# Kernel tuning notes

Hardware: AMD Instinct MI355X
Metric: run time of the kernel (lower is better)

## Reference

```python
import jax, jax.numpy as jnp
import numpy as np
from jax import lax

N, D, H, E = 8192, 1024, 4096, 8


def setup_inputs() -> dict:
    key = jax.random.key(0)
    ks = jax.random.split(key, 7)
    s = 0.02
    return {
        "x": jax.random.normal(ks[0], (N, D), dtype=jnp.float32),
        "Wr": jax.random.normal(ks[1], (E, D), dtype=jnp.float32) * s,
        "br": jnp.zeros((E,), dtype=jnp.float32),
        "Wup": jax.random.normal(ks[2], (E, H, D), dtype=jnp.float32) * s,
        "bup": jnp.zeros((E, H), dtype=jnp.float32),
        "Wdown": jax.random.normal(ks[3], (E, D, H), dtype=jnp.float32) * s,
        "bdown": jnp.zeros((E, D), dtype=jnp.float32),
    }


def reference(x, Wr, br, Wup, bup, Wdown, bdown):
    # Router: softmax over logits; only argmax is used (softmax is monotone,
    # argmax of softmax == argmax of logits).
    logits = x @ Wr.T + br            # [N, E]
    scores = jax.nn.softmax(logits, axis=-1)
    top1 = jnp.argmax(scores, axis=-1)  # [N] int

    out0 = jnp.zeros_like(x)

    def body(out, ew):
        i, Wu, bu, Wd, bd = ew
        h = jax.nn.silu(x @ Wu.T + bu)   # [N, H]
        y = h @ Wd.T + bd                # [N, D]
        out = jnp.where((top1 == i)[:, None], y, out)
        return out, None

    idx = jnp.arange(Wup.shape[0])
    out, _ = lax.scan(body, out0, (idx, Wup, bup, Wdown, bdown))
    return out
```

## Files before the change

### kernel.cpp

```cpp
#include <hip/hip_runtime.h>

#define NT 8192
#define DD 1024
#define HH 4096
#define EE 8

typedef __attribute__((ext_vector_type(8))) short short8;
typedef __attribute__((ext_vector_type(4))) float f32x4;

__device__ __forceinline__ unsigned short f2bf(float f) {
    unsigned int u = __float_as_uint(f);
    u += 0x7FFFu + ((u >> 16) & 1u);
    return (unsigned short)(u >> 16);
}

__device__ __forceinline__ void gload_lds16(const void* g, void* l) {
    __builtin_amdgcn_global_load_lds(
        (const __attribute__((address_space(1))) unsigned int*)g,
        (__attribute__((address_space(3))) unsigned int*)l, 16, 0, 0);
}

__global__ __launch_bounds__(256) void cvtw_kernel(const float* __restrict__ a,
                                                   const float* __restrict__ b,
                                                   unsigned short* __restrict__ da,
                                                   unsigned short* __restrict__ db) {
    const size_t half = (size_t)EE * HH * DD;
    size_t i = ((size_t)blockIdx.x * 256 + threadIdx.x) * 4;
    const float* s; unsigned short* d;
    if (i < half) { s = a + i; d = da + i; }
    else          { s = b + (i - half); d = db + (i - half); }
    float4 v = *(const float4*)s;
    ushort4 o;
    o.x = f2bf(v.x); o.y = f2bf(v.y); o.z = f2bf(v.z); o.w = f2bf(v.w);
    *(ushort4*)d = o;
}

__global__ __launch_bounds__(256) void router_kernel(const float* __restrict__ x,
                                                     const float* __restrict__ Wr,
                                                     const float* __restrict__ br,
                                                     int* __restrict__ counts,
                                                     int* __restrict__ tlist) {
    __shared__ float sW[EE * DD];
    const int t = threadIdx.x;
    for (int i = t; i < EE * DD / 4; i += 256)
        ((float4*)sW)[i] = ((const float4*)Wr)[i];
    __syncthreads();
    const int lane = t & 63;
    const int wv = t >> 6;
    const int token = blockIdx.x * 4 + wv;
    const float* xr = x + (size_t)token * DD;
    float acc[EE];
#pragma unroll
    for (int e = 0; e < EE; e++) acc[e] = 0.f;
    for (int k = lane; k < DD; k += 64) {
        float xv = xr[k];
#pragma unroll
        for (int e = 0; e < EE; e++) acc[e] += xv * sW[e * DD + k];
    }
#pragma unroll
    for (int off = 32; off > 0; off >>= 1) {
#pragma unroll
        for (int e = 0; e < EE; e++) acc[e] += __shfl_xor(acc[e], off);
    }
    if (lane == 0) {
        int best = 0;
        float bv = acc[0] + br[0];
#pragma unroll
        for (int e = 1; e < EE; e++) {
            float v = acc[e] + br[e];
            if (v > bv) { bv = v; best = e; }
        }
        int pos = atomicAdd(&counts[best], 1);
        tlist[best * NT + pos] = token;
    }
}

__global__ __launch_bounds__(256) void gather_kernel(const float* __restrict__ x,
                                                     const int* __restrict__ tlist,
                                                     const int* __restrict__ counts,
                                                     unsigned short* __restrict__ xg) {
    const int row = blockIdx.x * 4 + (threadIdx.x >> 6);
    const int lane = threadIdx.x & 63;
    int off[EE];
    int s = 0;
#pragma unroll
    for (int k = 0; k < EE; k++) { off[k] = s; s += counts[k]; }
    int e = 0;
#pragma unroll
    for (int k = 1; k < EE; k++)
        if (row >= off[k]) e = k;
    const int token = tlist[e * NT + row - off[e]];
    const float4* src = (const float4*)(x + (size_t)token * DD);
    ushort4* dst = (ushort4*)(xg + (size_t)row * DD);
#pragma unroll
    for (int it = 0; it < 4; it++) {
        float4 v = src[it * 64 + lane];
        ushort4 o;
        o.x = f2bf(v.x); o.y = f2bf(v.y); o.z = f2bf(v.z); o.w = f2bf(v.w);
        dst[it * 64 + lane] = o;
    }
}


__global__ __launch_bounds__(256) void up_gemm(const unsigned short* __restrict__ xg,
                                               const unsigned short* __restrict__ Wub,
                                               const float* __restrict__ bup,
                                               const int* __restrict__ counts,
                                               unsigned short* __restrict__ hbuf) {
    const int e = blockIdx.z;
    int off_e = 0, cnt;
    {
        int s = 0;
#pragma unroll
        for (int k = 0; k < EE; k++) { if (k == e) off_e = s; s += counts[k]; }
        cnt = counts[e];
    }
    const int m0 = blockIdx.y * 128;
    if (m0 >= cnt) return;
    const int n0 = blockIdx.x * 128;
    const int t = threadIdx.x;

    __shared__ unsigned short sA[128 * 32];
    __shared__ unsigned short sB[128 * 32];

    const int r0 = t >> 2;
    const int kc = (t & 3) ^ ((r0 >> 1) & 3);
    const int c1 = cnt - 1;
    int ra = m0 + r0;      if (ra > c1) ra = c1;
    int rb = m0 + 64 + r0; if (rb > c1) rb = c1;
    const unsigned short* gA0 = xg + (size_t)(off_e + ra) * DD + kc * 8;
    const unsigned short* gA1 = xg + (size_t)(off_e + rb) * DD + kc * 8;
    const unsigned short* gB0 = Wub + ((size_t)e * HH + n0 + r0) * DD + kc * 8;
    const unsigned short* gB1 = Wub + ((size_t)e * HH + n0 + 64 + r0) * DD + kc * 8;
    unsigned short* lA0 = sA + t * 8;
    unsigned short* lA1 = sA + (t + 256) * 8;
    unsigned short* lB0 = sB + t * 8;
    unsigned short* lB1 = sB + (t + 256) * 8;

    const int lane = t & 63;
    const int wm = ((t >> 6) & 1) * 64;
    const int wn = (t >> 7) * 64;
    const int mrow = lane & 15;
    const int kq = lane >> 4;
    const int slot = (kq ^ ((mrow >> 1) & 3)) * 8;

    f32x4 acc[4][4];
#pragma unroll
    for (int i = 0; i < 4; i++)
#pragma unroll
        for (int j = 0; j < 4; j++)
            acc[i][j] = (f32x4){0.f, 0.f, 0.f, 0.f};

    for (int kt = 0; kt < DD; kt += 32) {
        __syncthreads();
        gload_lds16(gA0 + kt, lA0);
        gload_lds16(gA1 + kt, lA1);
        gload_lds16(gB0 + kt, lB0);
        gload_lds16(gB1 + kt, lB1);
        __syncthreads();
        short8 a[4], b[4];
#pragma unroll
        for (int i = 0; i < 4; i++) {
            a[i] = *(const short8*)(sA + (wm + i * 16 + mrow) * 32 + slot);
            b[i] = *(const short8*)(sB + (wn + i * 16 + mrow) * 32 + slot);
        }
#pragma unroll
        for (int i = 0; i < 4; i++)
#pragma unroll
            for (int j = 0; j < 4; j++)
                acc[i][j] = __builtin_amdgcn_mfma_f32_16x16x32_bf16(a[i], b[j], acc[i][j], 0, 0, 0);
    }

    float bias[4];
#pragma unroll
    for (int j = 0; j < 4; j++) bias[j] = bup[e * HH + n0 + wn + j * 16 + mrow];
#pragma unroll
    for (int i = 0; i < 4; i++) {
#pragma unroll
        for (int r = 0; r < 4; r++) {
            int m = m0 + wm + i * 16 + kq * 4 + r;
            if (m < cnt) {
                unsigned short* hrow = hbuf + (size_t)(off_e + m) * HH + n0 + wn + mrow;
#pragma unroll
                for (int j = 0; j < 4; j++) {
                    float v = acc[i][j][r] + bias[j];
                    v = v / (1.f + __expf(-v));
                    hrow[j * 16] = f2bf(v);
                }
            }
        }
    }
}

__global__ __launch_bounds__(256) void down_gemm(const unsigned short* __restrict__ hbuf,
                                                 const unsigned short* __restrict__ Wdb,
                                                 const float* __restrict__ bdown,
                                                 const int* __restrict__ counts,
                                                 const int* __restrict__ tlist,
                                                 float* __restrict__ out) {
    const int e = blockIdx.z;
    int off_e = 0, cnt;
    {
        int s = 0;
#pragma unroll
        for (int k = 0; k < EE; k++) { if (k == e) off_e = s; s += counts[k]; }
        cnt = counts[e];
    }
    const int m0 = blockIdx.y * 128;
    if (m0 >= cnt) return;
    const int n0 = blockIdx.x * 128;
    const int t = threadIdx.x;

    __shared__ unsigned short sA[128 * 32];
    __shared__ unsigned short sB[128 * 32];

    const int r0 = t >> 2;
    const int kc = (t & 3) ^ ((r0 >> 1) & 3);
    const int c1 = cnt - 1;
    int ra = m0 + r0;      if (ra > c1) ra = c1;
    int rb = m0 + 64 + r0; if (rb > c1) rb = c1;
    const unsigned short* gA0 = hbuf + (size_t)(off_e + ra) * HH + kc * 8;
    const unsigned short* gA1 = hbuf + (size_t)(off_e + rb) * HH + kc * 8;
    const unsigned short* gB0 = Wdb + ((size_t)e * DD + n0 + r0) * HH + kc * 8;
    const unsigned short* gB1 = Wdb + ((size_t)e * DD + n0 + 64 + r0) * HH + kc * 8;
    unsigned short* lA0 = sA + t * 8;
    unsigned short* lA1 = sA + (t + 256) * 8;
    unsigned short* lB0 = sB + t * 8;
    unsigned short* lB1 = sB + (t + 256) * 8;

    const int lane = t & 63;
    const int wm = ((t >> 6) & 1) * 64;
    const int wn = (t >> 7) * 64;
    const int mrow = lane & 15;
    const int kq = lane >> 4;
    const int slot = (kq ^ ((mrow >> 1) & 3)) * 8;

    f32x4 acc[4][4];
#pragma unroll
    for (int i = 0; i < 4; i++)
#pragma unroll
        for (int j = 0; j < 4; j++)
            acc[i][j] = (f32x4){0.f, 0.f, 0.f, 0.f};

    for (int kt = 0; kt < HH; kt += 32) {
        __syncthreads();
        gload_lds16(gA0 + kt, lA0);
        gload_lds16(gA1 + kt, lA1);
        gload_lds16(gB0 + kt, lB0);
        gload_lds16(gB1 + kt, lB1);
        __syncthreads();
        short8 a[4], b[4];
#pragma unroll
        for (int i = 0; i < 4; i++) {
            a[i] = *(const short8*)(sA + (wm + i * 16 + mrow) * 32 + slot);
            b[i] = *(const short8*)(sB + (wn + i * 16 + mrow) * 32 + slot);
        }
#pragma unroll
        for (int i = 0; i < 4; i++)
#pragma unroll
            for (int j = 0; j < 4; j++)
                acc[i][j] = __builtin_amdgcn_mfma_f32_16x16x32_bf16(a[i], b[j], acc[i][j], 0, 0, 0);
    }

    const int* tl = tlist + e * NT;
    float bias[4];
#pragma unroll
    for (int j = 0; j < 4; j++) bias[j] = bdown[e * DD + n0 + wn + j * 16 + mrow];
#pragma unroll
    for (int i = 0; i < 4; i++) {
#pragma unroll
        for (int r = 0; r < 4; r++) {
            int m = m0 + wm + i * 16 + kq * 4 + r;
            if (m < cnt) {
                int token = tl[m];
                float* orow = out + (size_t)token * DD + n0 + wn + mrow;
#pragma unroll
                for (int j = 0; j < 4; j++)
                    orow[j * 16] = acc[i][j][r] + bias[j];
            }
        }
    }
}

extern "C" void kernel_launch(void* const* d_in, const int* in_sizes, int n_in,
                              void* d_out, int out_size, void* d_ws, size_t ws_size,
                              hipStream_t stream) {
    const float* x     = (const float*)d_in[0];
    const float* Wr    = (const float*)d_in[1];
    const float* br    = (const float*)d_in[2];
    const float* Wup   = (const float*)d_in[3];
    const float* bup   = (const float*)d_in[4];
    const float* Wdown = (const float*)d_in[5];
    const float* bdown = (const float*)d_in[6];
    float* out = (float*)d_out;

    char* w = (char*)d_ws;
    int* counts  = (int*)w;               w += 256;
    int* tlist   = (int*)w;               w += (size_t)EE * NT * 4;
    unsigned short* xg   = (unsigned short*)w;  w += (size_t)NT * DD * 2;
    unsigned short* hbuf = (unsigned short*)w;  w += (size_t)NT * HH * 2;
    unsigned short* Wub  = (unsigned short*)w;  w += (size_t)EE * HH * DD * 2;
    unsigned short* Wdb  = (unsigned short*)w;

    hipMemsetAsync(counts, 0, EE * sizeof(int), stream);

    cvtw_kernel<<<(2 * (size_t)EE * HH * DD) / 1024, 256, 0, stream>>>(Wup, Wdown, Wub, Wdb);
    router_kernel<<<NT / 4, 256, 0, stream>>>(x, Wr, br, counts, tlist);
    gather_kernel<<<NT / 4, 256, 0, stream>>>(x, tlist, counts, xg);

    dim3 gu(HH / 128, NT / 128, EE);
    up_gemm<<<gu, 256, 0, stream>>>(xg, Wub, bup, counts, hbuf);
    dim3 gd(DD / 128, NT / 128, EE);
    down_gemm<<<gd, 256, 0, stream>>>(hbuf, Wdb, bdown, counts, tlist, out);
}
```

Measured before the change: 659.0 us.

## Fuse fp32-to-bf16 weight conversion into GEMM loads and split-K the down GEMM

```diff
diff --git a/kernel.cpp b/kernel.cpp
--- a/kernel.cpp
+++ b/kernel.cpp
@@ -20,19 +20,13 @@
         (__attribute__((address_space(3))) unsigned int*)l, 16, 0, 0);
 }
 
-__global__ __launch_bounds__(256) void cvtw_kernel(const float* __restrict__ a,
-                                                   const float* __restrict__ b,
-                                                   unsigned short* __restrict__ da,
-                                                   unsigned short* __restrict__ db) {
-    const size_t half = (size_t)EE * HH * DD;
-    size_t i = ((size_t)blockIdx.x * 256 + threadIdx.x) * 4;
-    const float* s; unsigned short* d;
-    if (i < half) { s = a + i; d = da + i; }
-    else          { s = b + (i - half); d = db + (i - half); }
-    float4 v = *(const float4*)s;
-    ushort4 o;
-    o.x = f2bf(v.x); o.y = f2bf(v.y); o.z = f2bf(v.z); o.w = f2bf(v.w);
-    *(ushort4*)d = o;
+__device__ __forceinline__ void pack_store8(unsigned short* l, float4 a, float4 b) {
+    uint4 w;
+    w.x = (unsigned)f2bf(a.x) | ((unsigned)f2bf(a.y) << 16);
+    w.y = (unsigned)f2bf(a.z) | ((unsigned)f2bf(a.w) << 16);
+    w.z = (unsigned)f2bf(b.x) | ((unsigned)f2bf(b.y) << 16);
+    w.w = (unsigned)f2bf(b.z) | ((unsigned)f2bf(b.w) << 16);
+    *(uint4*)l = w;
 }
 
 __global__ __launch_bounds__(256) void router_kernel(const float* __restrict__ x,
@@ -103,7 +97,7 @@
 
 
 __global__ __launch_bounds__(256) void up_gemm(const unsigned short* __restrict__ xg,
-                                               const unsigned short* __restrict__ Wub,
+                                               const float* __restrict__ Wup,
                                                const float* __restrict__ bup,
                                                const int* __restrict__ counts,
                                                unsigned short* __restrict__ hbuf) {
@@ -124,18 +118,20 @@
     __shared__ unsigned short sB[128 * 32];
 
     const int r0 = t >> 2;
-    const int kc = (t & 3) ^ ((r0 >> 1) & 3);
+    const int kc = t & 3;
+    const int ksw = (r0 >> 1) & 3;
+    const int kcA = kc ^ ksw;
     const int c1 = cnt - 1;
     int ra = m0 + r0;      if (ra > c1) ra = c1;
     int rb = m0 + 64 + r0; if (rb > c1) rb = c1;
-    const unsigned short* gA0 = xg + (size_t)(off_e + ra) * DD + kc * 8;
-    const unsigned short* gA1 = xg + (size_t)(off_e + rb) * DD + kc * 8;
-    const unsigned short* gB0 = Wub + ((size_t)e * HH + n0 + r0) * DD + kc * 8;
-    const unsigned short* gB1 = Wub + ((size_t)e * HH + n0 + 64 + r0) * DD + kc * 8;
+    const unsigned short* gA0 = xg + (size_t)(off_e + ra) * DD + kcA * 8;
+    const unsigned short* gA1 = xg + (size_t)(off_e + rb) * DD + kcA * 8;
+    const float* gB0 = Wup + ((size_t)e * HH + n0 + r0) * DD + kc * 8;
+    const float* gB1 = Wup + ((size_t)e * HH + n0 + 64 + r0) * DD + kc * 8;
     unsigned short* lA0 = sA + t * 8;
     unsigned short* lA1 = sA + (t + 256) * 8;
-    unsigned short* lB0 = sB + t * 8;
-    unsigned short* lB1 = sB + (t + 256) * 8;
+    unsigned short* lB0 = sB + (r0 * 4 + (kc ^ ksw)) * 8;
+    unsigned short* lB1 = sB + ((r0 + 64) * 4 + (kc ^ ksw)) * 8;
 
     const int lane = t & 63;
     const int wm = ((t >> 6) & 1) * 64;
@@ -152,11 +148,15 @@
             acc[i][j] = (f32x4){0.f, 0.f, 0.f, 0.f};
 
     for (int kt = 0; kt < DD; kt += 32) {
+        float4 b00 = *(const float4*)(gB0 + kt);
+        float4 b01 = *(const float4*)(gB0 + kt + 4);
+        float4 b10 = *(const float4*)(gB1 + kt);
+        float4 b11 = *(const float4*)(gB1 + kt + 4);
         __syncthreads();
         gload_lds16(gA0 + kt, lA0);
         gload_lds16(gA1 + kt, lA1);
-        gload_lds16(gB0 + kt, lB0);
-        gload_lds16(gB1 + kt, lB1);
+        pack_store8(lB0, b00, b01);
+        pack_store8(lB1, b10, b11);
         __syncthreads();
         short8 a[4], b[4];
 #pragma unroll
@@ -193,12 +193,11 @@
 }
 
 __global__ __launch_bounds__(256) void down_gemm(const unsigned short* __restrict__ hbuf,
-                                                 const unsigned short* __restrict__ Wdb,
-                                                 const float* __restrict__ bdown,
+                                                 const float* __restrict__ Wdown,
                                                  const int* __restrict__ counts,
-                                                 const int* __restrict__ tlist,
-                                                 float* __restrict__ out) {
-    const int e = blockIdx.z;
+                                                 float* __restrict__ part) {
+    const int e = blockIdx.z >> 1;
+    const int sp = blockIdx.z & 1;
     int off_e = 0, cnt;
     {
         int s = 0;
@@ -215,18 +214,20 @@
     __shared__ unsigned short sB[128 * 32];
 
     const int r0 = t >> 2;
-    const int kc = (t & 3) ^ ((r0 >> 1) & 3);
+    const int kc = t & 3;
+    const int ksw = (r0 >> 1) & 3;
+    const int kcA = kc ^ ksw;
     const int c1 = cnt - 1;
     int ra = m0 + r0;      if (ra > c1) ra = c1;
     int rb = m0 + 64 + r0; if (rb > c1) rb = c1;
-    const unsigned short* gA0 = hbuf + (size_t)(off_e + ra) * HH + kc * 8;
-    const unsigned short* gA1 = hbuf + (size_t)(off_e + rb) * HH + kc * 8;
-    const unsigned short* gB0 = Wdb + ((size_t)e * DD + n0 + r0) * HH + kc * 8;
-    const unsigned short* gB1 = Wdb + ((size_t)e * DD + n0 + 64 + r0) * HH + kc * 8;
+    const unsigned short* gA0 = hbuf + (size_t)(off_e + ra) * HH + kcA * 8;
+    const unsigned short* gA1 = hbuf + (size_t)(off_e + rb) * HH + kcA * 8;
+    const float* gB0 = Wdown + ((size_t)e * DD + n0 + r0) * HH + kc * 8;
+    const float* gB1 = Wdown + ((size_t)e * DD + n0 + 64 + r0) * HH + kc * 8;
     unsigned short* lA0 = sA + t * 8;
     unsigned short* lA1 = sA + (t + 256) * 8;
-    unsigned short* lB0 = sB + t * 8;
-    unsigned short* lB1 = sB + (t + 256) * 8;
+    unsigned short* lB0 = sB + (r0 * 4 + (kc ^ ksw)) * 8;
+    unsigned short* lB1 = sB + ((r0 + 64) * 4 + (kc ^ ksw)) * 8;
 
     const int lane = t & 63;
     const int wm = ((t >> 6) & 1) * 64;
@@ -242,12 +243,18 @@
         for (int j = 0; j < 4; j++)
             acc[i][j] = (f32x4){0.f, 0.f, 0.f, 0.f};
 
-    for (int kt = 0; kt < HH; kt += 32) {
+    const int kbeg = sp * (HH / 2);
+    const int kend = kbeg + (HH / 2);
+    for (int kt = kbeg; kt < kend; kt += 32) {
+        float4 b00 = *(const float4*)(gB0 + kt);
+        float4 b01 = *(const float4*)(gB0 + kt + 4);
+        float4 b10 = *(const float4*)(gB1 + kt);
+        float4 b11 = *(const float4*)(gB1 + kt + 4);
         __syncthreads();
         gload_lds16(gA0 + kt, lA0);
         gload_lds16(gA1 + kt, lA1);
-        gload_lds16(gB0 + kt, lB0);
-        gload_lds16(gB1 + kt, lB1);
+        pack_store8(lB0, b00, b01);
+        pack_store8(lB1, b10, b11);
         __syncthreads();
         short8 a[4], b[4];
 #pragma unroll
@@ -262,23 +269,52 @@
                 acc[i][j] = __builtin_amdgcn_mfma_f32_16x16x32_bf16(a[i], b[j], acc[i][j], 0, 0, 0);
     }
 
-    const int* tl = tlist + e * NT;
-    float bias[4];
-#pragma unroll
-    for (int j = 0; j < 4; j++) bias[j] = bdown[e * DD + n0 + wn + j * 16 + mrow];
+    float* pbase = part + (size_t)sp * NT * DD;
 #pragma unroll
     for (int i = 0; i < 4; i++) {
 #pragma unroll
         for (int r = 0; r < 4; r++) {
             int m = m0 + wm + i * 16 + kq * 4 + r;
             if (m < cnt) {
-                int token = tl[m];
-                float* orow = out + (size_t)token * DD + n0 + wn + mrow;
+                float* prow = pbase + (size_t)(off_e + m) * DD + n0 + wn + mrow;
 #pragma unroll
                 for (int j = 0; j < 4; j++)
-                    orow[j * 16] = acc[i][j][r] + bias[j];
+                    prow[j * 16] = acc[i][j][r];
             }
         }
+    }
+}
+
+__global__ __launch_bounds__(256) void reduce_kernel(const float* __restrict__ part,
+                                                     const float* __restrict__ bdown,
+                                                     const int* __restrict__ counts,
+                                                     const int* __restrict__ tlist,
+                                                     float* __restrict__ out) {
+    const int row = blockIdx.x * 4 + (threadIdx.x >> 6);
+    const int lane = threadIdx.x & 63;
+    int off[EE];
+    int s = 0;
+#pragma unroll
+    for (int k = 0; k < EE; k++) { off[k] = s; s += counts[k]; }
+    int e = 0;
+#pragma unroll
+    for (int k = 1; k < EE; k++)
+        if (row >= off[k]) e = k;
+    const int token = tlist[e * NT + row - off[e]];
+    const float4* p0 = (const float4*)(part + (size_t)row * DD);
+    const float4* p1 = (const float4*)(part + (size_t)(NT + row) * DD);
+    const float4* bd = (const float4*)(bdown + (size_t)e * DD);
+    float4* o = (float4*)(out + (size_t)token * DD);
+#pragma unroll
+    for (int it = 0; it < 4; it++) {
+        int c = it * 64 + lane;
+        float4 a = p0[c], b = p1[c], g = bd[c];
+        float4 v;
+        v.x = a.x + b.x + g.x;
+        v.y = a.y + b.y + g.y;
+        v.z = a.z + b.z + g.z;
+        v.w = a.w + b.w + g.w;
+        o[c] = v;
     }
 }
 
@@ -295,21 +331,20 @@
     float* out = (float*)d_out;
 
     char* w = (char*)d_ws;
-    int* counts  = (int*)w;               w += 256;
-    int* tlist   = (int*)w;               w += (size_t)EE * NT * 4;
+    int* counts  = (int*)w;                     w += 256;
+    int* tlist   = (int*)w;                     w += (size_t)EE * NT * 4;
     unsigned short* xg   = (unsigned short*)w;  w += (size_t)NT * DD * 2;
     unsigned short* hbuf = (unsigned short*)w;  w += (size_t)NT * HH * 2;
-    unsigned short* Wub  = (unsigned short*)w;  w += (size_t)EE * HH * DD * 2;
-    unsigned short* Wdb  = (unsigned short*)w;
+    float* part = (float*)w;                    w += (size_t)2 * NT * DD * 4;
 
     hipMemsetAsync(counts, 0, EE * sizeof(int), stream);
 
-    cvtw_kernel<<<(2 * (size_t)EE * HH * DD) / 1024, 256, 0, stream>>>(Wup, Wdown, Wub, Wdb);
     router_kernel<<<NT / 4, 256, 0, stream>>>(x, Wr, br, counts, tlist);
     gather_kernel<<<NT / 4, 256, 0, stream>>>(x, tlist, counts, xg);
 
     dim3 gu(HH / 128, NT / 128, EE);
-    up_gemm<<<gu, 256, 0, stream>>>(xg, Wub, bup, counts, hbuf);
-    dim3 gd(DD / 128, NT / 128, EE);
-    down_gemm<<<gd, 256, 0, stream>>>(hbuf, Wdb, bdown, counts, tlist, out);
-}
+    up_gemm<<<gu, 256, 0, stream>>>(xg, Wup, bup, counts, hbuf);
+    dim3 gd(DD / 128, NT / 128, EE * 2);
+    down_gemm<<<gd, 256, 0, stream>>>(hbuf, Wdown, counts, part);
+    reduce_kernel<<<NT / 4, 256, 0, stream>>>(part, bdown, counts, tlist, out);
+}
```

Result: slower. 714.5 us (+8.4%).
